# Kernel tuning notes

Measured on AMD Instinct MI355X. Metric: run time of the kernel, lower is better.

Reference implementation:

```python
import jax, jax.numpy as jnp
import numpy as np

IN_FEATURES = 1024
OUT_FEATURES = 64
DEGREE = 3
NUM_KNOTS = 10
BATCH = 8192
K0 = NUM_KNOTS + DEGREE  # number of basis columns / control points per edge


def b_spline_basis(x, knots, degree):
    """Vectorized Cox-de Boor recursion.
    x: (..., ) values in [0,1]; knots: (K0+1,).
    Returns (..., K0) basis; last `degree` columns are zero-padded (matches
    control_points width of num_knots+degree as in the original module).
    """
    t = knots
    n0 = t.shape[0] - 1  # = K0 degree-0 intervals
    xe = x[..., None]
    basis = ((xe >= t[:-1]) & (xe < t[1:])).astype(x.dtype)  # (..., K0)
    for p in range(1, degree + 1):
        ti = t[: n0 - p]
        tip = t[p:n0]
        ti1 = t[1 : n0 - p + 1]
        tip1 = t[p + 1 : n0 + 1]
        d1 = jnp.where(tip - ti > 0, tip - ti, jnp.ones_like(ti))
        d2 = jnp.where(tip1 - ti1 > 0, tip1 - ti1, jnp.ones_like(ti1))
        left = jnp.where(tip - ti > 0, (xe - ti) / d1, 0.0) * basis[..., : n0 - p]
        right = jnp.where(tip1 - ti1 > 0, (tip1 - xe) / d2, 0.0) * basis[..., 1 : n0 - p + 1]
        new = left + right
        pad = jnp.zeros(x.shape + (p,), x.dtype)
        basis = jnp.concatenate([new, pad], axis=-1)
    return basis


def setup_inputs() -> dict:
    key = jax.random.key(0)
    k1, k2 = jax.random.split(key)
    x = jax.random.uniform(k1, (BATCH, IN_FEATURES), dtype=jnp.float32)
    knots = jnp.linspace(0.0, 1.0, NUM_KNOTS + DEGREE + 1, dtype=jnp.float32)
    control_points = jax.random.normal(k2, (OUT_FEATURES, IN_FEATURES, K0), dtype=jnp.float32)
    return {"x": x, "knots": knots, "control_points": control_points}


def reference(x, knots, control_points):
    # basis: (B, in, K0) computed once per input feature (original recomputes
    # it out_features times inside a double loop -- same math, fused here).
    basis = b_spline_basis(x, knots, DEGREE)
    # outputs[b, o] = sum_j sum_k basis[b, j, k] * control_points[o, j, k]
    return jnp.einsum("bjk,ojk->bo", basis, control_points)
```

## Files before the change

### kernel.cpp

```cpp
#include <hip/hip_runtime.h>
#include <hip/hip_bf16.h>
#include <stdint.h>

#define IN_F   1024
#define OUT_F  64
#define BATCH  8192
#define BM     256
#define NTHR   256
#define JSPLIT 32
#define JPB    (IN_F / JSPLIT)
#define JC     4
#define NCH    (JPB / JC)
#define BT_B   (JC * 2048)
#define X_B    (BM * JC * 4)
#define BUF_B  (BT_B + X_B)
#define NBUF   3
#define OUTSZ  (BATCH * OUT_F)

typedef __attribute__((ext_vector_type(8)))  short short8;
typedef __attribute__((ext_vector_type(16))) float f32x16;

__device__ __forceinline__ void gll16(const void* g, void* l) {
    __builtin_amdgcn_global_load_lds(
        (const __attribute__((address_space(1))) uint32_t*)g,
        (__attribute__((address_space(3))) uint32_t*)l,
        16, 0, 0);
}

__global__ void kan_prep(const float* __restrict__ cp, __hip_bfloat16* __restrict__ bt) {
    int j = blockIdx.x * 4 + (threadIdx.x >> 6);
    int o = threadIdx.x & 63;
    const float* src = cp + ((size_t)o * IN_F + j) * 13;
    float v[16];
#pragma unroll
    for (int k = 0; k < 10; ++k) v[k] = src[k];
#pragma unroll
    for (int k = 10; k < 16; ++k) v[k] = 0.0f;
    __hip_bfloat16* dst = bt + (size_t)j * 1024;
#pragma unroll
    for (int kh = 0; kh < 2; ++kh)
#pragma unroll
        for (int e = 0; e < 8; ++e)
            dst[kh * 512 + o * 8 + e] = __float2bfloat16(v[kh * 8 + e]);
}

__device__ __forceinline__ short8 afrag(float xv, int c0) {
    const float t = xv * 13.0f;
    float uu;
    asm("v_fract_f32 %0, %1" : "=v"(uu) : "v"(t));
    const int m = (int)t;
    const float u2 = uu * uu;
    const float omu = 1.0f - uu;
    const float o2 = omu * omu;
    const float B3 = u2 * (uu * (1.0f / 6.0f));
    const float B0 = o2 * (omu * (1.0f / 6.0f));
    const float B1 = __builtin_fmaf(u2, __builtin_fmaf(uu, 0.5f, -1.0f), 2.0f / 3.0f);
    const float B2 = 1.0f - B0 - B1 - B3;
    uint32_t P01, P23;
    asm("v_cvt_pk_bf16_f32 %0, %1, %2" : "=v"(P01) : "v"(B0), "v"(B1));
    asm("v_cvt_pk_bf16_f32 %0, %1, %2" : "=v"(P23) : "v"(B2), "v"(B3));
    const uint64_t V = ((uint64_t)P23 << 32) | (uint64_t)P01;
    const int p = (m << 4) - c0;
    const uint64_t sl = V << ((uint32_t)p & 63);
    const uint64_t sr = V >> ((uint32_t)(-p) & 63);
    const uint64_t t0 = (p < 0) ? sr : sl;
    const uint64_t q0 = ((uint32_t)(p + 63) < 127u) ? t0 : 0ull;
    const uint64_t t1 = (p < 64) ? sr : sl;
    const uint64_t q1 = ((uint32_t)(p - 16) < 112u) ? t1 : 0ull;
    union { uint64_t q[2]; short8 s; } cv;
    cv.q[0] = q0; cv.q[1] = q1;
    return cv.s;
}

template<bool PART>
__launch_bounds__(NTHR, 4)
__global__ void kan_main(const float* __restrict__ x,
                         const __hip_bfloat16* __restrict__ bt,
                         void* __restrict__ outp) {
    __shared__ __attribute__((aligned(16))) char lds[NBUF * BUF_B];

    const int tid   = threadIdx.x;
    const int w     = tid >> 6;
    const int lane  = tid & 63;
    const int l31   = lane & 31;
    const int khalf = lane >> 5;
    const int c0    = 48 + (khalf << 7);

    const int r0 = blockIdx.x * BM;
    const int j0 = blockIdx.y * JPB;

    const char* btg = (const char*)bt + (size_t)j0 * 2048 + (size_t)tid * 16;
    const char* xgt = (const char*)(x + (size_t)(r0 + tid) * IN_F + j0);
    const int   wofs = w << 10;

#define STAGE(ch, bi) do {                                        \
        char* base_ = lds + (bi) * BUF_B;                         \
        const char* gb_ = btg + (size_t)(ch) * BT_B;              \
        gll16(gb_,        base_ + wofs);                          \
        gll16(gb_ + 4096, base_ + 4096 + wofs);                   \
        gll16(xgt + (ch) * (JC * 4), base_ + BT_B + wofs);        \
    } while (0)

#define COMPUTE(bi) do {                                                      \
        const char* base = lds + (bi) * BUF_B;                                \
        float xa0[4], xa1[4];                                                 \
        const char* xr = base + BT_B + (((w << 6) + l31) << 4);               \
        *(float4*)xa0 = *(const float4*)(xr);              \
        *(float4*)xa1 = *(const float4*)(xr + 512);     \
        const char* bbb = base + (khalf << 10) + l31 * 16;                    \
        _Pragma("unroll")                                                     \
        for (int jl = 0; jl < JC; ++jl) {                                     \
            const short8 b0 = *(const short8*)(bbb + jl * 2048);              \
            const short8 b1 = *(const short8*)(bbb + jl * 2048 + 512);        \
            const short8 a0 = afrag(xa0[jl], c0);                             \
            const short8 a1 = afrag(xa1[jl], c0);                             \
            acc00 = __builtin_amdgcn_mfma_f32_32x32x16_bf16(a0, b0, acc00, 0, 0, 0); \
            acc01 = __builtin_amdgcn_mfma_f32_32x32x16_bf16(a0, b1, acc01, 0, 0, 0); \
            acc10 = __builtin_amdgcn_mfma_f32_32x32x16_bf16(a1, b0, acc10, 0, 0, 0); \
            acc11 = __builtin_amdgcn_mfma_f32_32x32x16_bf16(a1, b1, acc11, 0, 0, 0); \
        }                                                                     \
    } while (0)

    f32x16 acc00, acc01, acc10, acc11;
#pragma unroll
    for (int i = 0; i < 16; ++i) {
        acc00[i] = 0.0f; acc01[i] = 0.0f; acc10[i] = 0.0f; acc11[i] = 0.0f;
    }

    STAGE(0, 0);
    STAGE(1, 1);

    int bi = 0;
#pragma unroll 1
    for (int ch = 0; ch < NCH - 1; ++ch) {
        asm volatile("s_waitcnt vmcnt(3)" ::: "memory");
        __builtin_amdgcn_s_barrier();
        __builtin_amdgcn_sched_barrier(0);
        if (ch + 2 < NCH) {
            int nb = bi + 2; if (nb >= NBUF) nb -= NBUF;
            STAGE(ch + 2, nb);
        }
        COMPUTE(bi);
        bi = (bi + 1 == NBUF) ? 0 : bi + 1;
    }
    asm volatile("s_waitcnt vmcnt(0)" ::: "memory");
    __builtin_amdgcn_s_barrier();
    __builtin_amdgcn_sched_barrier(0);
    COMPUTE(bi);
#undef STAGE
#undef COMPUTE

    if (PART) {
        __hip_bfloat16* op = (__hip_bfloat16*)outp + (size_t)blockIdx.y * OUTSZ;
#pragma unroll
        for (int r = 0; r < 16; ++r) {
            const int crow = (r & 3) + 8 * (r >> 2) + 4 * khalf;
            __hip_bfloat16* p0 = op + (size_t)(r0 + (w << 6) + crow) * OUT_F;
            __hip_bfloat16* p1 = p0 + 32 * OUT_F;
            p0[l31]      = __float2bfloat16(acc00[r]);
            p0[l31 + 32] = __float2bfloat16(acc01[r]);
            p1[l31]      = __float2bfloat16(acc10[r]);
            p1[l31 + 32] = __float2bfloat16(acc11[r]);
        }
    } else {
        float* op = (float*)outp;
#pragma unroll
        for (int r = 0; r < 16; ++r) {
            const int crow = (r & 3) + 8 * (r >> 2) + 4 * khalf;
            float* p0 = op + (size_t)(r0 + (w << 6) + crow) * OUT_F;
            float* p1 = p0 + 32 * OUT_F;
            atomicAdd(p0 + l31,      acc00[r]);
            atomicAdd(p0 + l31 + 32, acc01[r]);
            atomicAdd(p1 + l31,      acc10[r]);
            atomicAdd(p1 + l31 + 32, acc11[r]);
        }
    }
}

__global__ void kan_reduce(const __hip_bfloat16* __restrict__ part,
                           float* __restrict__ out) {
    const int i = (blockIdx.x * 256 + threadIdx.x) * 8;
    float s[8] = {0, 0, 0, 0, 0, 0, 0, 0};
#pragma unroll
    for (int b = 0; b < JSPLIT; ++b) {
        const short8 v = *(const short8*)(part + (size_t)b * OUTSZ + i);
#pragma unroll
        for (int e = 0; e < 8; ++e) {
            union { uint32_t u; float f; } c;
            c.u = ((uint32_t)(uint16_t)v[e]) << 16;
            s[e] += c.f;
        }
    }
    float4 lo = {s[0], s[1], s[2], s[3]}, hi = {s[4], s[5], s[6], s[7]};
    *(float4*)(out + i)     = lo;
    *(float4*)(out + i + 4) = hi;
}

extern "C" void kernel_launch(void* const* d_in, const int* in_sizes, int n_in,
                              void* d_out, int out_size, void* d_ws, size_t ws_size,
                              hipStream_t stream) {
    const float* x  = (const float*)d_in[0];
    const float* cp = (const float*)d_in[2];
    float* out = (float*)d_out;
    __hip_bfloat16* bt   = (__hip_bfloat16*)d_ws;
    __hip_bfloat16* part = (__hip_bfloat16*)((char*)d_ws + 2u * 1024u * 1024u);

    const size_t need = 2u * 1024u * 1024u + (size_t)JSPLIT * OUTSZ * 2u;
    const bool use_part = ws_size >= need;

    kan_prep<<<dim3(IN_F / 4), dim3(256), 0, stream>>>(cp, bt);
    if (use_part) {
        kan_main<true><<<dim3(BATCH / BM, JSPLIT), dim3(NTHR), 0, stream>>>(x, bt, (void*)part);
        kan_reduce<<<dim3(OUTSZ / 2048), dim3(256), 0, stream>>>(part, out);
    } else {
        hipMemsetAsync(d_out, 0, (size_t)out_size * sizeof(float), stream);
        kan_main<false><<<dim3(BATCH / BM, JSPLIT), dim3(NTHR), 0, stream>>>(x, bt, (void*)d_out);
    }
}
```

Measured before the change: 49.30 us.

## Replace per-element B-spline evaluation with quantized LDS lookup table, double-buffer pipeline

```diff
diff --git a/kernel.cpp b/kernel.cpp
--- a/kernel.cpp
+++ b/kernel.cpp
@@ -14,7 +14,8 @@
 #define BT_B   (JC * 2048)
 #define X_B    (BM * JC * 4)
 #define BUF_B  (BT_B + X_B)
-#define NBUF   3
+#define TBL_B  (14 * 64 * 32)
+#define LDS_T  (TBL_B + 2 * BUF_B)
 #define OUTSZ  (BATCH * OUT_F)
 
 typedef __attribute__((ext_vector_type(8)))  short short8;
@@ -44,65 +45,72 @@
             dst[kh * 512 + o * 8 + e] = __float2bfloat16(v[kh * 8 + e]);
 }
 
-__device__ __forceinline__ short8 afrag(float xv, int c0) {
-    const float t = xv * 13.0f;
-    float uu;
-    asm("v_fract_f32 %0, %1" : "=v"(uu) : "v"(t));
-    const int m = (int)t;
-    const float u2 = uu * uu;
-    const float omu = 1.0f - uu;
-    const float o2 = omu * omu;
-    const float B3 = u2 * (uu * (1.0f / 6.0f));
-    const float B0 = o2 * (omu * (1.0f / 6.0f));
-    const float B1 = __builtin_fmaf(u2, __builtin_fmaf(uu, 0.5f, -1.0f), 2.0f / 3.0f);
-    const float B2 = 1.0f - B0 - B1 - B3;
-    uint32_t P01, P23;
-    asm("v_cvt_pk_bf16_f32 %0, %1, %2" : "=v"(P01) : "v"(B0), "v"(B1));
-    asm("v_cvt_pk_bf16_f32 %0, %1, %2" : "=v"(P23) : "v"(B2), "v"(B3));
-    const uint64_t V = ((uint64_t)P23 << 32) | (uint64_t)P01;
-    const int p = (m << 4) - c0;
-    const uint64_t sl = V << ((uint32_t)p & 63);
-    const uint64_t sr = V >> ((uint32_t)(-p) & 63);
-    const uint64_t t0 = (p < 0) ? sr : sl;
-    const uint64_t q0 = ((uint32_t)(p + 63) < 127u) ? t0 : 0ull;
-    const uint64_t t1 = (p < 64) ? sr : sl;
-    const uint64_t q1 = ((uint32_t)(p - 16) < 112u) ? t1 : 0ull;
-    union { uint64_t q[2]; short8 s; } cv;
-    cv.q[0] = q0; cv.q[1] = q1;
-    return cv.s;
-}
-
 template<bool PART>
-__launch_bounds__(NTHR, 4)
+__launch_bounds__(NTHR, 3)
 __global__ void kan_main(const float* __restrict__ x,
                          const __hip_bfloat16* __restrict__ bt,
                          void* __restrict__ outp) {
-    __shared__ __attribute__((aligned(16))) char lds[NBUF * BUF_B];
+    __shared__ __attribute__((aligned(16))) char lds[LDS_T];
 
     const int tid   = threadIdx.x;
     const int w     = tid >> 6;
     const int lane  = tid & 63;
     const int l31   = lane & 31;
     const int khalf = lane >> 5;
-    const int c0    = 48 + (khalf << 7);
 
     const int r0 = blockIdx.x * BM;
     const int j0 = blockIdx.y * JPB;
+
+    for (int e = tid; e < 14 * 64; e += NTHR) {
+        const int m = e >> 6, u6 = e & 63;
+        const float uu = (u6 + 0.5f) * (1.0f / 64.0f);
+        const float u2 = uu * uu;
+        const float omu = 1.0f - uu;
+        const float o2 = omu * omu;
+        const float B3 = u2 * (uu * (1.0f / 6.0f));
+        const float B0 = o2 * (omu * (1.0f / 6.0f));
+        const float B1 = __builtin_fmaf(u2, __builtin_fmaf(uu, 0.5f, -1.0f), 2.0f / 3.0f);
+        const float B2 = 1.0f - B0 - B1 - B3;
+        uint32_t P01, P23;
+        asm("v_cvt_pk_bf16_f32 %0, %1, %2" : "=v"(P01) : "v"(B0), "v"(B1));
+        asm("v_cvt_pk_bf16_f32 %0, %1, %2" : "=v"(P23) : "v"(B2), "v"(B3));
+        const uint64_t V = ((uint64_t)P23 << 32) | (uint64_t)P01;
+        const int slot = (m << 6) | (u6 ^ (m & 3));
+#pragma unroll
+        for (int h = 0; h < 2; ++h) {
+            const int c0 = 48 + (h << 7);
+            const int p = (m << 4) - c0;
+            const uint64_t sl = V << ((uint32_t)p & 63);
+            const uint64_t sr = V >> ((uint32_t)(-p) & 63);
+            const uint64_t t0 = (p < 0) ? sr : sl;
+            const uint64_t q0 = ((uint32_t)(p + 63) < 127u) ? t0 : 0ull;
+            const uint64_t t1 = (p < 64) ? sr : sl;
+            const uint64_t q1 = ((uint32_t)(p - 16) < 112u) ? t1 : 0ull;
+            uint64_t* d = (uint64_t*)(lds + slot * 32 + h * 16);
+            d[0] = q0; d[1] = q1;
+        }
+    }
 
     const char* btg = (const char*)bt + (size_t)j0 * 2048 + (size_t)tid * 16;
     const char* xgt = (const char*)(x + (size_t)(r0 + tid) * IN_F + j0);
     const int   wofs = w << 10;
 
 #define STAGE(ch, bi) do {                                        \
-        char* base_ = lds + (bi) * BUF_B;                         \
+        char* base_ = lds + TBL_B + (bi) * BUF_B;                 \
         const char* gb_ = btg + (size_t)(ch) * BT_B;              \
         gll16(gb_,        base_ + wofs);                          \
         gll16(gb_ + 4096, base_ + 4096 + wofs);                   \
         gll16(xgt + (ch) * (JC * 4), base_ + BT_B + wofs);        \
     } while (0)
 
+#define AFRAG(xv) ({                                              \
+        const float t128_ = (xv) * 832.0f;           \
+        const int i_ = (int)t128_;                 \
+        const int s_ = (i_ ^ ((i_ >> 6) & 3)) << 5;               \
+        *(const short8*)(lds + s_ + (khalf << 4)); })
+
 #define COMPUTE(bi) do {                                                      \
-        const char* base = lds + (bi) * BUF_B;                                \
+        const char* base = lds + TBL_B + (bi) * BUF_B;                        \
         float xa0[4], xa1[4];                                                 \
         const char* xr = base + BT_B + (((w << 6) + l31) << 4);               \
         *(float4*)xa0 = *(const float4*)(xr);              \
@@ -112,8 +120,8 @@
         for (int jl = 0; jl < JC; ++jl) {                                     \
             const short8 b0 = *(const short8*)(bbb + jl * 2048);              \
             const short8 b1 = *(const short8*)(bbb + jl * 2048 + 512);        \
-            const short8 a0 = afrag(xa0[jl], c0);                             \
-            const short8 a1 = afrag(xa1[jl], c0);                             \
+            const short8 a0 = AFRAG(xa0[jl]);                                 \
+            const short8 a1 = AFRAG(xa1[jl]);                                 \
             acc00 = __builtin_amdgcn_mfma_f32_32x32x16_bf16(a0, b0, acc00, 0, 0, 0); \
             acc01 = __builtin_amdgcn_mfma_f32_32x32x16_bf16(a0, b1, acc01, 0, 0, 0); \
             acc10 = __builtin_amdgcn_mfma_f32_32x32x16_bf16(a1, b0, acc10, 0, 0, 0); \
@@ -129,25 +137,26 @@
 
     STAGE(0, 0);
     STAGE(1, 1);
-
-    int bi = 0;
+    __syncthreads();
+
+    int cur = 0;
 #pragma unroll 1
-    for (int ch = 0; ch < NCH - 1; ++ch) {
-        asm volatile("s_waitcnt vmcnt(3)" ::: "memory");
-        __builtin_amdgcn_s_barrier();
-        __builtin_amdgcn_sched_barrier(0);
+    for (int ch = 0; ch < NCH; ++ch) {
+        if (ch >= 2) {
+            asm volatile("s_waitcnt vmcnt(3)" ::: "memory");
+            __builtin_amdgcn_s_barrier();
+            __builtin_amdgcn_sched_barrier(0);
+        }
+        COMPUTE(cur);
         if (ch + 2 < NCH) {
-            int nb = bi + 2; if (nb >= NBUF) nb -= NBUF;
-            STAGE(ch + 2, nb);
-        }
-        COMPUTE(bi);
-        bi = (bi + 1 == NBUF) ? 0 : bi + 1;
-    }
-    asm volatile("s_waitcnt vmcnt(0)" ::: "memory");
-    __builtin_amdgcn_s_barrier();
-    __builtin_amdgcn_sched_barrier(0);
-    COMPUTE(bi);
+            __builtin_amdgcn_s_barrier();
+            __builtin_amdgcn_sched_barrier(0);
+            STAGE(ch + 2, cur);
+        }
+        cur ^= 1;
+    }
 #undef STAGE
+#undef AFRAG
 #undef COMPUTE
 
     if (PART) {
```

Result: faster. 45.19 us (-8.3%).
